# Optimization experiments

Hardware: AMD Instinct MI355X
Metric: run time of the kernel (lower is better)

## Reference

```python
import jax, jax.numpy as jnp
import numpy as np

BS, N_CTX, N_HEADS, WIDTH = 2, 2048, 8, 32
N_TOK = 512


def setup_inputs() -> dict:
    key = jax.random.key(0)
    kq, kk, kv, ki = jax.random.split(key, 4)
    q = jax.random.normal(kq, (BS, N_CTX, N_HEADS, WIDTH), dtype=jnp.float32)
    k = jax.random.normal(kk, (BS, N_CTX, N_HEADS, WIDTH), dtype=jnp.float32)
    v = jax.random.normal(kv, (BS, N_CTX, N_HEADS, WIDTH), dtype=jnp.float32)
    indx = jnp.sort(jax.random.randint(ki, (N_TOK,), 0, N_CTX, dtype=jnp.int64))
    return {"q": q, "k": k, "v": v, "indx": indx}


def reference(q, k, v, indx):
    # q, k, v: (bs, n_ctx, n_heads, width); indx: (n_tok,) token ids to attend over
    n_tok = indx.shape[0]
    scale = jnp.float32(1.0 / np.sqrt(n_tok))
    qg = q[:, indx]  # (bs, n_tok, h, w) -- gathered tokens (t axis in torch code)
    kg = k[:, indx]  # (bs, n_tok, h, w) -- gathered tokens (s axis in torch code)
    vg = v[:, indx]  # (bs, n_tok, h, w)
    # L1 distance scores: ww[b,s,t,h] = scale * sum_w |q[b,indx[t],h,w] - k[b,indx[s],h,w]|
    diff = jnp.abs(qg[:, None, :, :, :] - kg[:, :, None, :, :])  # (bs, s, t, h, w)
    scores = -scale * jnp.sum(diff, axis=-1)  # (bs, s, t, h)
    attn = jax.nn.softmax(scores, axis=2)  # softmax over t (matches torch softmax(-1) on (b,h,s,t))
    # out[b,s,h,w] = sum_t attn[b,s,t,h] * v[b,indx[t],h,w]
    out = jnp.einsum('bsth,bthw->bshw', attn, vg)
    return out
```

## Files before the change

kernel.cpp:

```cpp
#include <hip/hip_runtime.h>

#define BS   2
#define NCTX 2048
#define NH   8
#define WD   32
#define NTOK 512

static constexpr float SCALE = 0.04419417382415922f;


__device__ __forceinline__ void load8(const float* __restrict__ base, int tok,
                                      float4 dst[4]) {
  const float4* p = (const float4*)(base + (size_t)tok * (NH * WD));
#pragma unroll
  for (int i = 0; i < 4; ++i) dst[i] = p[i];
}

__device__ __forceinline__ void body(const float4 qd[4], const float4 vd[4],
                                     const float kg[16], float& l, float acc[16]) {
  float d0 = 0.f, d1 = 0.f, d2 = 0.f, d3 = 0.f;
#pragma unroll
  for (int i = 0; i < 4; ++i) {
    d0 += fabsf(kg[4*i+0] - qd[i].x);
    d1 += fabsf(kg[4*i+1] - qd[i].y);
    d2 += fabsf(kg[4*i+2] - qd[i].z);
    d3 += fabsf(kg[4*i+3] - qd[i].w);
  }
  float d = (d0 + d1) + (d2 + d3);
  d += __shfl_xor(d, 32, 64);
  float p = __expf(-SCALE * d);
  l += p;
#pragma unroll
  for (int i = 0; i < 4; ++i) {
    acc[4*i+0] = fmaf(p, vd[i].x, acc[4*i+0]);
    acc[4*i+1] = fmaf(p, vd[i].y, acc[4*i+1]);
    acc[4*i+2] = fmaf(p, vd[i].z, acc[4*i+2]);
    acc[4*i+3] = fmaf(p, vd[i].w, acc[4*i+3]);
  }
}

__global__ void __launch_bounds__(1024, 4)
l1attn_v2(const float* __restrict__ q, const float* __restrict__ k,
          const float* __restrict__ v, const int* __restrict__ indx,
          float* __restrict__ out) {
  __shared__ int   indxS[NTOK];
  __shared__ float accS[32 * 33];
  __shared__ float lS[32];

  const int tid = threadIdx.x;

  if (tid < NTOK) indxS[tid] = indx[tid];
  for (int i = tid; i < 32 * 33; i += 1024) accS[i] = 0.f;
  if (tid < 32) lS[tid] = 0.f;
  __syncthreads();

  const int wave  = __builtin_amdgcn_readfirstlane(tid >> 6);
  const int lane  = tid & 63;
  const int whalf = lane >> 5;
  const int r     = lane & 31;

  const int bh = blockIdx.x >> 4;
  const int g  = blockIdx.x & 15;
  const int b  = bh >> 3;
  const int h  = bh & 7;
  const int s  = g * 32 + r;

  const float* qb = q + ((size_t)b * NCTX * NH + h) * WD + whalf * 16;
  const float* vb = v + ((size_t)b * NCTX * NH + h) * WD + whalf * 16;
  const float* kb = k + ((size_t)b * NCTX * NH + h) * WD + whalf * 16;

  float kg[16];
  {
    const float4* kr = (const float4*)(kb + (size_t)indxS[s] * (NH * WD));
#pragma unroll
    for (int i = 0; i < 4; ++i) {
      float4 t = kr[i];
      kg[4*i+0] = t.x; kg[4*i+1] = t.y; kg[4*i+2] = t.z; kg[4*i+3] = t.w;
    }
  }

  float acc[16];
#pragma unroll
  for (int i = 0; i < 16; ++i) acc[i] = 0.f;
  float l = 0.f;

  const int jb = wave * 32;

  float4 q0[4], v0[4], q1[4], v1[4];
  int tokB = indxS[jb + 1];
  load8(qb, indxS[jb], q0);
  load8(vb, indxS[jb], v0);

  for (int jj = 0; jj < 32; jj += 2) {
    const int tokC = indxS[jb + ((jj + 2) & 31)];
    const int tokD = indxS[jb + ((jj + 3) & 31)];

    load8(qb, tokB, q1);
    load8(vb, tokB, v1);
    body(q0, v0, kg, l, acc);

    load8(qb, tokC, q0);
    load8(vb, tokC, v0);
    body(q1, v1, kg, l, acc);

    tokB = tokD;
  }

#pragma unroll
  for (int i = 0; i < 16; ++i)
    atomicAdd(&accS[r * 33 + whalf * 16 + i], acc[i]);
  if (whalf == 0) atomicAdd(&lS[r], l);
  __syncthreads();

  {
    const int rr = tid >> 5;
    const int ww = tid & 31;
    const float res = accS[rr * 33 + ww] / lS[rr];
    const int ss = g * 32 + rr;
    out[(((size_t)b * NTOK + ss) * NH + h) * WD + ww] = res;
  }
}

extern "C" void kernel_launch(void* const* d_in, const int* in_sizes, int n_in,
                              void* d_out, int out_size, void* d_ws, size_t ws_size,
                              hipStream_t stream) {
  const float* q    = (const float*)d_in[0];
  const float* k    = (const float*)d_in[1];
  const float* v    = (const float*)d_in[2];
  const int*   indx = (const int*)d_in[3];
  float*       out  = (float*)d_out;

  dim3 grid(256), block(1024);
  hipLaunchKernelGGL(l1attn_v2, grid, block, 0, stream, q, k, v, indx, out);
}
```

Baseline: 55.46 us.

## Load wave-uniform Q/V rows via scalar loads and split token loop across blocks

Each lane now owns a whole query row of width 32, so the Q and V rows for a token are the same for every lane in a wave. They are fetched with s_load_dwordx16 into scalar registers instead of per-lane vector loads, which also removes the cross-half shuffle. The token range is split between two blocks that write partial sums and denominators to workspace, and a second combine kernel merges them and divides. The cost is higher per-lane register use, a synchronous s_waitcnt after every load with no prefetch overlap, and an extra kernel launch plus a workspace round trip.

```diff
diff --git a/kernel.cpp b/kernel.cpp
--- a/kernel.cpp
+++ b/kernel.cpp
@@ -1,6 +1,5 @@
 #include <hip/hip_runtime.h>
 
-#define BS   2
 #define NCTX 2048
 #define NH   8
 #define WD   32
@@ -8,117 +7,132 @@
 
 static constexpr float SCALE = 0.04419417382415922f;
 
+typedef float f32x16 __attribute__((ext_vector_type(16)));
 
-__device__ __forceinline__ void load8(const float* __restrict__ base, int tok,
-                                      float4 dst[4]) {
-  const float4* p = (const float4*)(base + (size_t)tok * (NH * WD));
-#pragma unroll
-  for (int i = 0; i < 4; ++i) dst[i] = p[i];
-}
-
-__device__ __forceinline__ void body(const float4 qd[4], const float4 vd[4],
-                                     const float kg[16], float& l, float acc[16]) {
-  float d0 = 0.f, d1 = 0.f, d2 = 0.f, d3 = 0.f;
-#pragma unroll
-  for (int i = 0; i < 4; ++i) {
-    d0 += fabsf(kg[4*i+0] - qd[i].x);
-    d1 += fabsf(kg[4*i+1] - qd[i].y);
-    d2 += fabsf(kg[4*i+2] - qd[i].z);
-    d3 += fabsf(kg[4*i+3] - qd[i].w);
-  }
-  float d = (d0 + d1) + (d2 + d3);
-  d += __shfl_xor(d, 32, 64);
-  float p = __expf(-SCALE * d);
-  l += p;
-#pragma unroll
-  for (int i = 0; i < 4; ++i) {
-    acc[4*i+0] = fmaf(p, vd[i].x, acc[4*i+0]);
-    acc[4*i+1] = fmaf(p, vd[i].y, acc[4*i+1]);
-    acc[4*i+2] = fmaf(p, vd[i].z, acc[4*i+2]);
-    acc[4*i+3] = fmaf(p, vd[i].w, acc[4*i+3]);
-  }
-}
-
-__global__ void __launch_bounds__(1024, 4)
-l1attn_v2(const float* __restrict__ q, const float* __restrict__ k,
-          const float* __restrict__ v, const int* __restrict__ indx,
-          float* __restrict__ out) {
+template<int JPW, bool PARTIAL>
+__global__ __launch_bounds__(1024, 4) void l1attn_main(
+    const float* __restrict__ q, const float* __restrict__ k,
+    const float* __restrict__ v, const int* __restrict__ indx,
+    float* __restrict__ dst ) {
   __shared__ int   indxS[NTOK];
-  __shared__ float accS[32 * 33];
-  __shared__ float lS[32];
+  __shared__ float accS[64 * 33];
+  __shared__ float lS[64];
 
   const int tid = threadIdx.x;
-
   if (tid < NTOK) indxS[tid] = indx[tid];
-  for (int i = tid; i < 32 * 33; i += 1024) accS[i] = 0.f;
-  if (tid < 32) lS[tid] = 0.f;
+  for (int i = tid; i < 64 * 33; i += 1024) accS[i] = 0.f;
+  if (tid < 64) lS[tid] = 0.f;
   __syncthreads();
 
-  const int wave  = __builtin_amdgcn_readfirstlane(tid >> 6);
-  const int lane  = tid & 63;
-  const int whalf = lane >> 5;
-  const int r     = lane & 31;
+  const int wave = __builtin_amdgcn_readfirstlane(tid >> 6);
+  const int lane = tid & 63;
 
-  const int bh = blockIdx.x >> 4;
-  const int g  = blockIdx.x & 15;
-  const int b  = bh >> 3;
-  const int h  = bh & 7;
-  const int s  = g * 32 + r;
+  int pr, jbase;
+  if (PARTIAL) { pr = blockIdx.x >> 1; jbase = ((blockIdx.x & 1) * 16 + wave) * 16; }
+  else         { pr = blockIdx.x;      jbase = wave * 32; }
+  const int plane = pr >> 3;
+  const int rg    = pr & 7;
+  const int b     = plane >> 3;
+  const int h     = plane & 7;
 
-  const float* qb = q + ((size_t)b * NCTX * NH + h) * WD + whalf * 16;
-  const float* vb = v + ((size_t)b * NCTX * NH + h) * WD + whalf * 16;
-  const float* kb = k + ((size_t)b * NCTX * NH + h) * WD + whalf * 16;
+  const float* qb = q + ((size_t)b * NCTX * NH + h) * WD;
+  const float* vb = v + ((size_t)b * NCTX * NH + h) * WD;
+  const float* kb = k + ((size_t)b * NCTX * NH + h) * WD;
 
-  float kg[16];
+  float kg[32];
   {
+    const int s = rg * 64 + lane;
     const float4* kr = (const float4*)(kb + (size_t)indxS[s] * (NH * WD));
 #pragma unroll
-    for (int i = 0; i < 4; ++i) {
+    for (int i = 0; i < 8; ++i) {
       float4 t = kr[i];
       kg[4*i+0] = t.x; kg[4*i+1] = t.y; kg[4*i+2] = t.z; kg[4*i+3] = t.w;
     }
   }
 
-  float acc[16];
+  float acc[32];
 #pragma unroll
-  for (int i = 0; i < 16; ++i) acc[i] = 0.f;
+  for (int i = 0; i < 32; ++i) acc[i] = 0.f;
   float l = 0.f;
 
-  const int jb = wave * 32;
+  int tok = __builtin_amdgcn_readfirstlane(indxS[jbase]);
+  for (int jj = 0; jj < JPW; ++jj) {
+    const int tokn =
+        __builtin_amdgcn_readfirstlane(indxS[jbase + ((jj + 1) & (JPW - 1))]);
+    const float* qp = qb + (size_t)tok * (NH * WD);
+    const float* vp = vb + (size_t)tok * (NH * WD);
 
-  float4 q0[4], v0[4], q1[4], v1[4];
-  int tokB = indxS[jb + 1];
-  load8(qb, indxS[jb], q0);
-  load8(vb, indxS[jb], v0);
+    f32x16 q0, q1, v0, v1;
+    asm volatile(
+        "s_load_dwordx16 %0, %4, 0x0\n\t"
+        "s_load_dwordx16 %1, %4, 0x40\n\t"
+        "s_load_dwordx16 %2, %5, 0x0\n\t"
+        "s_load_dwordx16 %3, %5, 0x40\n\t"
+        "s_waitcnt lgkmcnt(0)"
+        : "=&s"(q0), "=&s"(q1), "=&s"(v0), "=&s"(v1)
+        : "s"(qp), "s"(vp));
 
-  for (int jj = 0; jj < 32; jj += 2) {
-    const int tokC = indxS[jb + ((jj + 2) & 31)];
-    const int tokD = indxS[jb + ((jj + 3) & 31)];
-
-    load8(qb, tokB, q1);
-    load8(vb, tokB, v1);
-    body(q0, v0, kg, l, acc);
-
-    load8(qb, tokC, q0);
-    load8(vb, tokC, v0);
-    body(q1, v1, kg, l, acc);
-
-    tokB = tokD;
+    float d0, d1, d2, d3;
+    d0 = fabsf(q0[0] - kg[0]);
+    d1 = fabsf(q0[1] - kg[1]);
+    d2 = fabsf(q0[2] - kg[2]);
+    d3 = fabsf(q0[3] - kg[3]);
+#pragma unroll
+    for (int i = 1; i < 4; ++i) {
+      d0 += fabsf(q0[4*i+0] - kg[4*i+0]);
+      d1 += fabsf(q0[4*i+1] - kg[4*i+1]);
+      d2 += fabsf(q0[4*i+2] - kg[4*i+2]);
+      d3 += fabsf(q0[4*i+3] - kg[4*i+3]);
+    }
+#pragma unroll
+    for (int i = 0; i < 4; ++i) {
+      d0 += fabsf(q1[4*i+0] - kg[16+4*i+0]);
+      d1 += fabsf(q1[4*i+1] - kg[16+4*i+1]);
+      d2 += fabsf(q1[4*i+2] - kg[16+4*i+2]);
+      d3 += fabsf(q1[4*i+3] - kg[16+4*i+3]);
+    }
+    const float d = (d0 + d1) + (d2 + d3);
+    const float p = __expf(-SCALE * d);
+    l += p;
+#pragma unroll
+    for (int i = 0; i < 16; ++i) {
+      acc[i]      = fmaf(p, v0[i], acc[i]);
+      acc[16 + i] = fmaf(p, v1[i], acc[16 + i]);
+    }
+    tok = tokn;
   }
 
 #pragma unroll
-  for (int i = 0; i < 16; ++i)
-    atomicAdd(&accS[r * 33 + whalf * 16 + i], acc[i]);
-  if (whalf == 0) atomicAdd(&lS[r], l);
+  for (int w = 0; w < 32; ++w) atomicAdd(&accS[lane * 33 + w], acc[w]);
+  atomicAdd(&lS[lane], l);
   __syncthreads();
 
-  {
-    const int rr = tid >> 5;
-    const int ww = tid & 31;
-    const float res = accS[rr * 33 + ww] / lS[rr];
-    const int ss = g * 32 + rr;
-    out[(((size_t)b * NTOK + ss) * NH + h) * WD + ww] = res;
+  if (PARTIAL) {
+    float* wsB = dst + (size_t)blockIdx.x * 2176;
+    for (int i = tid; i < 64 * 33; i += 1024) wsB[i] = accS[i];
+    if (tid < 64) wsB[64 * 33 + tid] = lS[tid];
+  } else {
+#pragma unroll
+    for (int idx = tid; idx < 2048; idx += 1024) {
+      const int r = idx >> 5, w = idx & 31;
+      dst[(((size_t)b * NTOK + rg * 64 + r) * NH + h) * WD + w] =
+          accS[r * 33 + w] / lS[r];
+    }
   }
+}
+
+__global__ __launch_bounds__(1024) void l1attn_combine(
+    const float* __restrict__ ws, float* __restrict__ out) {
+  const int gid = blockIdx.x * 1024 + threadIdx.x;
+  const int w  = gid & 31;
+  const int r  = (gid >> 5) & 63;
+  const int pr = gid >> 11;
+  const int b  = pr >> 6, h = (pr >> 3) & 7, rg = pr & 7;
+  const float* pa = ws + (size_t)(2 * pr)     * 2176;
+  const float* pb = ws + (size_t)(2 * pr + 1) * 2176;
+  const float acc = pa[r * 33 + w] + pb[r * 33 + w];
+  const float lsum = pa[2112 + r] + pb[2112 + r];
+  out[(((size_t)b * NTOK + rg * 64 + r) * NH + h) * WD + w] = acc / lsum;
 }
 
 extern "C" void kernel_launch(void* const* d_in, const int* in_sizes, int n_in,
@@ -130,6 +144,14 @@
   const int*   indx = (const int*)d_in[3];
   float*       out  = (float*)d_out;
 
-  dim3 grid(256), block(1024);
-  hipLaunchKernelGGL(l1attn_v2, grid, block, 0, stream, q, k, v, indx, out);
+  const size_t need = (size_t)256 * 2176 * sizeof(float);
+  if (ws_size >= need) {
+    hipLaunchKernelGGL((l1attn_main<16, true>), dim3(256), dim3(1024), 0, stream,
+                       q, k, v, indx, (float*)d_ws);
+    hipLaunchKernelGGL(l1attn_combine, dim3(256), dim3(1024), 0, stream,
+                       (const float*)d_ws, out);
+  } else {
+    hipLaunchKernelGGL((l1attn_main<32, false>), dim3(128), dim3(1024), 0, stream,
+                       q, k, v, indx, out);
+  }
 }
```

Result: slower. 60.36 us (+8.8%).
